# Performance work log

Hardware: AMD Instinct MI355X
Metric: run time of the kernel (lower is better)

The kernel has to match this reference:

```python
import jax, jax.numpy as jnp
import numpy as np

H, W_GRID = 64, 64          # grid size -> N = 4096 stations
CTX, HID = 512, 2048        # ctx_features, hidden_size
K, BATCH = 8, 8             # nearest_k, batch
N = H * W_GRID


def _build_neighbors(seed=0):
    """Mimics __init__: for each grid cell, k nearest cells by Euclidean grid
    distance, with similarity exp(-||f_i - f_j||) from a random scalar field."""
    rng = np.random.default_rng(seed)
    field = rng.standard_normal((H, W_GRID)).astype(np.float32)
    ii, jj = np.meshgrid(np.arange(H), np.arange(W_GRID), indexing='ij')
    coords = np.stack([ii.ravel(), jj.ravel()], axis=1).astype(np.float32)  # [N,2]
    d2 = ((coords[:, None, :] - coords[None, :, :]) ** 2).sum(-1).astype(np.float32)
    np.fill_diagonal(d2, np.inf)                      # exclude self (m!=i or n!=j)
    nn_idx = np.argsort(d2, axis=1)[:, :K].astype(np.int32)   # [N,K] flat ids
    f = field.ravel()
    sim = np.exp(-np.abs(f[:, None] - f[nn_idx])).astype(np.float32)  # [N,K]
    return nn_idx, sim


def setup_inputs() -> dict:
    key = jax.random.key(0)
    k1, k2 = jax.random.split(key)
    contextual_val = jax.random.normal(k1, (BATCH, H, W_GRID, CTX), dtype=jnp.float32)
    W = jax.random.normal(k2, (CTX, HID), dtype=jnp.float32)
    nn_idx, sim = _build_neighbors(seed=0)
    return {
        "contextual_val": contextual_val,
        "W": W,
        "nn_idx": jnp.asarray(nn_idx),
        "sim": jnp.asarray(sim),
    }


def reference(contextual_val, W, nn_idx, sim):
    # res[b, n, :] = sum_k sim[n, k] * (x[b, nn_idx[n, k], :] @ W)
    # By linearity: aggregate neighbor features with similarity weights first,
    # then apply the shared projection W once (same math, one GEMM).
    B = contextual_val.shape[0]
    x = contextual_val.reshape(B, N, CTX)          # [B, N, C]
    gathered = x[:, nn_idx]                        # [B, N, K, C] neighbor gather
    agg = jnp.einsum('nk,bnkc->bnc', sim, gathered)  # weighted scatter-add
    out = jnp.einsum('bnc,ch->bnh', agg, W)          # shared small matmul
    return out.reshape(B, H, W_GRID, HID)
```

## Files before the change

kernel.cpp:

```cpp
#include <hip/hip_runtime.h>
#include <cstdint>

#define CTX 512
#define HID 2048
#define NCELL 4096
#define M_TOT 32768

typedef __bf16 bf16;
typedef __attribute__((ext_vector_type(8))) __bf16 bf16x8;
typedef __attribute__((ext_vector_type(4))) float f32x4;

__device__ __align__(16) unsigned short g_agg[(size_t)M_TOT * CTX];
__device__ __align__(16) unsigned short g_WT[(size_t)HID * CTX];
__device__ int g_flag;

__device__ __forceinline__ float bf2f(unsigned short u) {
  union { unsigned int i; float f; } c; c.i = ((unsigned int)u) << 16; return c.f;
}
__device__ __forceinline__ unsigned short f2bf(float f) {
  union { float f; unsigned int i; } c; c.f = f;
  unsigned int u = c.i;
  u += 0x7fffu + ((u >> 16) & 1u);
  return (unsigned short)(u >> 16);
}
__device__ __forceinline__ float lo16(unsigned int w) {
  union { unsigned int i; float f; } c; c.i = w << 16; return c.f;
}
__device__ __forceinline__ float hi16(unsigned int w) {
  union { unsigned int i; float f; } c; c.i = w & 0xffff0000u; return c.f;
}

__device__ __forceinline__ void gload_lds16(const void* g, void* s) {
  __builtin_amdgcn_global_load_lds(
      (const __attribute__((address_space(1))) void*)g,
      (__attribute__((address_space(3))) void*)s, 16, 0, 0);
}

__global__ void detect_dtype(const unsigned short* __restrict__ x, int* flagp) {
  __shared__ int cnt;
  if (threadIdx.x == 0) cnt = 0;
  __syncthreads();
  const uint4 v = ((const uint4*)x)[threadIdx.x];
  unsigned int w[4] = {v.x, v.y, v.z, v.w};
  int c = 0;
#pragma unroll
  for (int i = 0; i < 4; ++i) {
    unsigned int lo = w[i] & 0xffffu, hi = w[i] >> 16;
    c += (((lo >> 7) & 0xffu) >= 0xF8u);
    c += (((hi >> 7) & 0xffu) >= 0xF8u);
  }
  atomicAdd(&cnt, c);
  __syncthreads();
  if (threadIdx.x == 0) *flagp = (cnt > 8) ? 1 : 0;
}

__global__ void transpose_w(const void* __restrict__ Wv,
                            unsigned short* __restrict__ wt,
                            const int* __restrict__ flagp) {
  const int isf32 = *flagp;
  const int t  = threadIdx.x;
  const int h  = blockIdx.x * 64 + (t & 63);
  const int c0 = (blockIdx.y * 4 + (t >> 6)) * 8;
  float e[8];
  if (isf32) {
    const float* Wf = (const float*)Wv;
#pragma unroll
    for (int j = 0; j < 8; ++j) e[j] = Wf[(size_t)(c0 + j) * HID + h];
  } else {
    const unsigned short* Wb = (const unsigned short*)Wv;
#pragma unroll
    for (int j = 0; j < 8; ++j) e[j] = bf2f(Wb[(size_t)(c0 + j) * HID + h]);
  }
  uint4 o;
  o.x = (unsigned int)f2bf(e[0]) | ((unsigned int)f2bf(e[1]) << 16);
  o.y = (unsigned int)f2bf(e[2]) | ((unsigned int)f2bf(e[3]) << 16);
  o.z = (unsigned int)f2bf(e[4]) | ((unsigned int)f2bf(e[5]) << 16);
  o.w = (unsigned int)f2bf(e[6]) | ((unsigned int)f2bf(e[7]) << 16);
  *(uint4*)&wt[(size_t)h * CTX + c0] = o;
}

__global__ void gather_agg_k(const void* __restrict__ xv,
                             const int* __restrict__ nn_idx,
                             const void* __restrict__ simv,
                             unsigned short* __restrict__ agg,
                             const int* __restrict__ flagp) {
  const int isf32 = *flagp;
  const int bid  = blockIdx.x;
  const int sb   = (bid & 7) * 1024 + (bid >> 3);
  const int m    = sb * 4 + (threadIdx.x >> 6);
  const int lane = threadIdx.x & 63;
  const int b    = m >> 12;
  const int n    = m & (NCELL - 1);

  float a[8] = {0, 0, 0, 0, 0, 0, 0, 0};
  if (isf32) {
    const int clo = lane * 4;
    const int chi = 256 + lane * 4;
    const float* xf = (const float*)xv;
    const float* sf = (const float*)simv;
#pragma unroll
    for (int k = 0; k < 8; ++k) {
      const int   idx = nn_idx[n * 8 + k];
      const float wgt = sf[n * 8 + k];
      const float* p  = xf + (size_t)(b * NCELL + idx) * CTX;
      const float4 v0 = *(const float4*)(p + clo);
      const float4 v1 = *(const float4*)(p + chi);
      a[0] += wgt * v0.x; a[1] += wgt * v0.y; a[2] += wgt * v0.z; a[3] += wgt * v0.w;
      a[4] += wgt * v1.x; a[5] += wgt * v1.y; a[6] += wgt * v1.z; a[7] += wgt * v1.w;
    }
    uint2 olo, ohi;
    olo.x = (unsigned int)f2bf(a[0]) | ((unsigned int)f2bf(a[1]) << 16);
    olo.y = (unsigned int)f2bf(a[2]) | ((unsigned int)f2bf(a[3]) << 16);
    ohi.x = (unsigned int)f2bf(a[4]) | ((unsigned int)f2bf(a[5]) << 16);
    ohi.y = (unsigned int)f2bf(a[6]) | ((unsigned int)f2bf(a[7]) << 16);
    *(uint2*)&agg[(size_t)m * CTX + clo] = olo;
    *(uint2*)&agg[(size_t)m * CTX + chi] = ohi;
  } else {
    const int c0 = lane * 8;
    const unsigned short* xb = (const unsigned short*)xv;
    const unsigned short* sb16 = (const unsigned short*)simv;
#pragma unroll
    for (int k = 0; k < 8; ++k) {
      const int   idx = nn_idx[n * 8 + k];
      const float wgt = bf2f(sb16[n * 8 + k]);
      const uint4 v = *(const uint4*)(xb + ((size_t)(b * NCELL + idx) * CTX + c0));
      a[0] += wgt * lo16(v.x); a[1] += wgt * hi16(v.x);
      a[2] += wgt * lo16(v.y); a[3] += wgt * hi16(v.y);
      a[4] += wgt * lo16(v.z); a[5] += wgt * hi16(v.z);
      a[6] += wgt * lo16(v.w); a[7] += wgt * hi16(v.w);
    }
    uint4 o;
    o.x = (unsigned int)f2bf(a[0]) | ((unsigned int)f2bf(a[1]) << 16);
    o.y = (unsigned int)f2bf(a[2]) | ((unsigned int)f2bf(a[3]) << 16);
    o.z = (unsigned int)f2bf(a[4]) | ((unsigned int)f2bf(a[5]) << 16);
    o.w = (unsigned int)f2bf(a[6]) | ((unsigned int)f2bf(a[7]) << 16);
    *(uint4*)&agg[(size_t)m * CTX + c0] = o;
  }
}

#define CS_STR 132
__global__ __launch_bounds__(256) void gemm_bt(const unsigned short* __restrict__ agg,
                                               const unsigned short* __restrict__ wt,
                                               void* __restrict__ outv,
                                               const int* __restrict__ flagp) {
  __shared__ __align__(16) char smem[65536];
  float* Cs = (float*)smem;

  const int tid  = threadIdx.x;
  const int wave = tid >> 6;
  const int lane = tid & 63;
  const int l16  = lane & 15;
  const int quad = lane >> 4;

  const int bid = blockIdx.x;
  const int swz = (bid & 7) * 512 + (bid >> 3);
  const int gn0 = (swz & 15) * 128;
  const int gm0 = (swz >> 4) * 128;

  const int wm = (wave & 1) * 64;
  const int wn = (wave >> 1) * 64;

  f32x4 acc[4][4] = {};

  const int srow = lane >> 3;
  const int l8   = lane & 7;

#define STAGE(b, kt)                                                          \
  {                                                                           \
    bf16* As_ = (bf16*)(smem + (b) * 32768);                                  \
    bf16* Bs_ = (bf16*)(smem + (b) * 32768 + 16384);                          \
    _Pragma("unroll")                                                         \
    for (int i = 0; i < 4; ++i) {                                             \
      const int chunk = wave * 4 + i;                                         \
      const int row   = chunk * 8 + srow;                                     \
      const int csw   = (l8 * 8) ^ ((row & 7) << 3);                          \
      gload_lds16(&agg[(size_t)(gm0 + row) * CTX + (kt) + csw],               \
                  &As_[chunk * 512]);                                         \
      gload_lds16(&wt[(size_t)(gn0 + row) * CTX + (kt) + csw],                \
                  &Bs_[chunk * 512]);                                         \
    }                                                                         \
  }

  STAGE(0, 0);

  for (int t = 0; t < 8; ++t) {
    if (t < 7) {
      STAGE((t + 1) & 1, (t + 1) * 64);
      asm volatile("s_waitcnt vmcnt(8)" ::: "memory");
    } else {
      asm volatile("s_waitcnt vmcnt(0)" ::: "memory");
    }
    __builtin_amdgcn_s_barrier();
    __builtin_amdgcn_sched_barrier(0);

    const bf16* A = (const bf16*)(smem + (t & 1) * 32768);
    const bf16* B = (const bf16*)(smem + (t & 1) * 32768 + 16384);

#pragma unroll
    for (int s = 0; s < 2; ++s) {
      bf16x8 af[4], bfr[4];
#pragma unroll
      for (int mi = 0; mi < 4; ++mi) {
        const int r = wm + mi * 16 + l16;
        af[mi] = *(const bf16x8*)&A[r * 64 + (((s * 4 + quad) * 8) ^ ((r & 7) << 3))];
      }
#pragma unroll
      for (int ni = 0; ni < 4; ++ni) {
        const int r = wn + ni * 16 + l16;
        bfr[ni] = *(const bf16x8*)&B[r * 64 + (((s * 4 + quad) * 8) ^ ((r & 7) << 3))];
      }
      __builtin_amdgcn_s_setprio(1);
#pragma unroll
      for (int mi = 0; mi < 4; ++mi)
#pragma unroll
        for (int ni = 0; ni < 4; ++ni)
          acc[mi][ni] = __builtin_amdgcn_mfma_f32_16x16x32_bf16(
              af[mi], bfr[ni], acc[mi][ni], 0, 0, 0);
      __builtin_amdgcn_s_setprio(0);
    }
    __builtin_amdgcn_s_barrier();
    __builtin_amdgcn_sched_barrier(0);
  }
#undef STAGE

  const int isf32 = *flagp;
  if (isf32) {
    float* out = (float*)outv;
#pragma unroll
    for (int h = 0; h < 2; ++h) {
      __syncthreads();
      if ((wave & 1) == h) {
#pragma unroll
        for (int mi = 0; mi < 4; ++mi)
#pragma unroll
          for (int r = 0; r < 4; ++r) {
            const int lr = mi * 16 + quad * 4 + r;
#pragma unroll
            for (int ni = 0; ni < 4; ++ni)
              Cs[lr * CS_STR + wn + ni * 16 + l16] = acc[mi][ni][r];
          }
      }
      __syncthreads();
#pragma unroll
      for (int p = 0; p < 8; ++p) {
        const int r  = p * 8 + (tid >> 5);
        const int c4 = (tid & 31) * 4;
        const f32x4 v = *(const f32x4*)&Cs[r * CS_STR + c4];
        *(f32x4*)&out[(size_t)(gm0 + h * 64 + r) * HID + gn0 + c4] = v;
      }
    }
  } else {
    unsigned short* out = (unsigned short*)outv;
#pragma unroll
    for (int mi = 0; mi < 4; ++mi)
#pragma unroll
      for (int r = 0; r < 4; ++r) {
        const size_t row = (size_t)(gm0 + wm + mi * 16 + quad * 4 + r);
#pragma unroll
        for (int ni = 0; ni < 4; ++ni)
          out[row * HID + gn0 + wn + ni * 16 + l16] = f2bf(acc[mi][ni][r]);
      }
  }
}

extern "C" void kernel_launch(void* const* d_in, const int* in_sizes, int n_in,
                              void* d_out, int out_size, void* d_ws, size_t ws_size,
                              hipStream_t stream) {
  const void* x   = d_in[0];
  const void* W   = d_in[1];
  const int*  nn  = (const int*)d_in[2];
  const void* sim = d_in[3];

  const size_t wt_bytes  = (size_t)HID * CTX * 2;
  const size_t agg_bytes = (size_t)M_TOT * CTX * 2;
  const size_t need      = wt_bytes + agg_bytes + 16;

  unsigned short *wt, *agg; int* flagp;
  if (ws_size >= need) {
    wt    = (unsigned short*)d_ws;
    agg   = (unsigned short*)((char*)d_ws + wt_bytes);
    flagp = (int*)((char*)d_ws + wt_bytes + agg_bytes);
  } else {
    void *p0, *p1, *p2;
    hipGetSymbolAddress(&p0, HIP_SYMBOL(g_WT));
    hipGetSymbolAddress(&p1, HIP_SYMBOL(g_agg));
    hipGetSymbolAddress(&p2, HIP_SYMBOL(g_flag));
    wt = (unsigned short*)p0; agg = (unsigned short*)p1; flagp = (int*)p2;
  }

  detect_dtype<<<1, 256, 0, stream>>>((const unsigned short*)x, flagp);
  transpose_w<<<dim3(HID / 64, CTX / 32), 256, 0, stream>>>(W, wt, flagp);
  gather_agg_k<<<dim3(M_TOT / 4), 256, 0, stream>>>(x, nn, sim, agg, flagp);
  gemm_bt<<<dim3((HID / 128) * (M_TOT / 128)), 256, 0, stream>>>(agg, wt, d_out, flagp);
}
```

Before: 405.6 us.

## Enlarge GEMM tile to 256x256 with 512 threads and interleaved prefetch

The bf16 MFMA GEMM moves from 128x128 tiles with 4 waves to 256x256 tiles with 8 waves, using 128 KB of dynamic LDS as two buffers. The aim is to raise arithmetic intensity and cut how often each block re-reads the agg and W tiles from global memory. Next-stage global-to-LDS loads are now split into four pieces and spread between MFMA groups, so memory traffic overlaps with compute. In exchange, 128 accumulator registers per lane and the large LDS footprint allow only one block per CU, and the grid shrinks to 1024 blocks, which may weaken latency hiding and leave a tail imbalance across CUs.

```diff
diff --git a/kernel.cpp b/kernel.cpp
--- a/kernel.cpp
+++ b/kernel.cpp
@@ -138,121 +138,123 @@
   }
 }
 
-#define CS_STR 132
-__global__ __launch_bounds__(256) void gemm_bt(const unsigned short* __restrict__ agg,
-                                               const unsigned short* __restrict__ wt,
-                                               void* __restrict__ outv,
-                                               const int* __restrict__ flagp) {
-  __shared__ __align__(16) char smem[65536];
-  float* Cs = (float*)smem;
+__global__ __launch_bounds__(512, 2) void gemm_bt(const unsigned short* __restrict__ agg,
+                                                  const unsigned short* __restrict__ wt,
+                                                  void* __restrict__ outv,
+                                                  const int* __restrict__ flagp) {
+  extern __shared__ char smem[];
 
   const int tid  = threadIdx.x;
   const int wave = tid >> 6;
   const int lane = tid & 63;
   const int l16  = lane & 15;
   const int quad = lane >> 4;
-
-  const int bid = blockIdx.x;
-  const int swz = (bid & 7) * 512 + (bid >> 3);
-  const int gn0 = (swz & 15) * 128;
-  const int gm0 = (swz >> 4) * 128;
-
-  const int wm = (wave & 1) * 64;
-  const int wn = (wave >> 1) * 64;
-
-  f32x4 acc[4][4] = {};
-
   const int srow = lane >> 3;
   const int l8   = lane & 7;
 
-#define STAGE(b, kt)                                                          \
+  const int bid = blockIdx.x;
+  const int swz = (bid & 7) * 128 + (bid >> 3);
+  const int gn0 = (swz & 7) * 256;
+  const int gm0 = (swz >> 3) * 256;
+
+  const int wm = (wave & 1) * 128;
+  const int wn = (wave >> 1) * 64;
+
+  f32x4 acc[8][4] = {};
+
+#define STAGE2(bsel, kt, j)                                                   \
   {                                                                           \
-    bf16* As_ = (bf16*)(smem + (b) * 32768);                                  \
-    bf16* Bs_ = (bf16*)(smem + (b) * 32768 + 16384);                          \
-    _Pragma("unroll")                                                         \
-    for (int i = 0; i < 4; ++i) {                                             \
-      const int chunk = wave * 4 + i;                                         \
-      const int row   = chunk * 8 + srow;                                     \
-      const int csw   = (l8 * 8) ^ ((row & 7) << 3);                          \
-      gload_lds16(&agg[(size_t)(gm0 + row) * CTX + (kt) + csw],               \
-                  &As_[chunk * 512]);                                         \
-      gload_lds16(&wt[(size_t)(gn0 + row) * CTX + (kt) + csw],                \
-                  &Bs_[chunk * 512]);                                         \
-    }                                                                         \
-  }
-
-  STAGE(0, 0);
+    const int chunk = wave * 4 + (j);                                         \
+    const int row   = chunk * 8 + srow;                                       \
+    const int csw   = (l8 * 8) ^ ((row & 7) << 3);                            \
+    gload_lds16(&agg[(size_t)(gm0 + row) * CTX + (kt) + csw],                 \
+                smem + (bsel) * 65536 + chunk * 1024);                        \
+    gload_lds16(&wt[(size_t)(gn0 + row) * CTX + (kt) + csw],                  \
+                smem + (bsel) * 65536 + 32768 + chunk * 1024);                \
+  }
+
+#pragma unroll
+  for (int j = 0; j < 4; ++j) STAGE2(0, 0, j);
 
   for (int t = 0; t < 8; ++t) {
-    if (t < 7) {
-      STAGE((t + 1) & 1, (t + 1) * 64);
-      asm volatile("s_waitcnt vmcnt(8)" ::: "memory");
-    } else {
-      asm volatile("s_waitcnt vmcnt(0)" ::: "memory");
-    }
+    const int c = t & 1;
+    __builtin_amdgcn_sched_barrier(0);
     __builtin_amdgcn_s_barrier();
     __builtin_amdgcn_sched_barrier(0);
-
-    const bf16* A = (const bf16*)(smem + (t & 1) * 32768);
-    const bf16* B = (const bf16*)(smem + (t & 1) * 32768 + 16384);
+    if (t < 7) STAGE2(c ^ 1, (t + 1) * 64, 0);
+    if (t < 7) asm volatile("s_waitcnt vmcnt(2)" ::: "memory");
+    else       asm volatile("s_waitcnt vmcnt(0)" ::: "memory");
+    __builtin_amdgcn_sched_barrier(0);
+    __builtin_amdgcn_s_barrier();
+    __builtin_amdgcn_sched_barrier(0);
+
+    const char* Ab = smem + c * 65536;
+    const char* Bb = Ab + 32768;
 
 #pragma unroll
     for (int s = 0; s < 2; ++s) {
-      bf16x8 af[4], bfr[4];
-#pragma unroll
-      for (int mi = 0; mi < 4; ++mi) {
-        const int r = wm + mi * 16 + l16;
-        af[mi] = *(const bf16x8*)&A[r * 64 + (((s * 4 + quad) * 8) ^ ((r & 7) << 3))];
-      }
+      bf16x8 bfv[4];
 #pragma unroll
       for (int ni = 0; ni < 4; ++ni) {
         const int r = wn + ni * 16 + l16;
-        bfr[ni] = *(const bf16x8*)&B[r * 64 + (((s * 4 + quad) * 8) ^ ((r & 7) << 3))];
-      }
-      __builtin_amdgcn_s_setprio(1);
-#pragma unroll
-      for (int mi = 0; mi < 4; ++mi)
-#pragma unroll
-        for (int ni = 0; ni < 4; ++ni)
-          acc[mi][ni] = __builtin_amdgcn_mfma_f32_16x16x32_bf16(
-              af[mi], bfr[ni], acc[mi][ni], 0, 0, 0);
-      __builtin_amdgcn_s_setprio(0);
+        bfv[ni] = *(const bf16x8*)(Bb + r * 128 +
+                                   2 * ((s * 32 + quad * 8) ^ ((r & 7) << 3)));
+      }
+#pragma unroll
+      for (int h = 0; h < 2; ++h) {
+        bf16x8 af[4];
+#pragma unroll
+        for (int mi2 = 0; mi2 < 4; ++mi2) {
+          const int r = wm + (h * 4 + mi2) * 16 + l16;
+          af[mi2] = *(const bf16x8*)(Ab + r * 128 +
+                                     2 * ((s * 32 + quad * 8) ^ ((r & 7) << 3)));
+        }
+        if (t < 7 && (s * 2 + h) < 3) STAGE2(c ^ 1, (t + 1) * 64, s * 2 + h + 1);
+        __builtin_amdgcn_s_setprio(1);
+#pragma unroll
+        for (int mi2 = 0; mi2 < 4; ++mi2)
+#pragma unroll
+          for (int ni = 0; ni < 4; ++ni)
+            acc[h * 4 + mi2][ni] = __builtin_amdgcn_mfma_f32_16x16x32_bf16(
+                af[mi2], bfv[ni], acc[h * 4 + mi2][ni], 0, 0, 0);
+        __builtin_amdgcn_s_setprio(0);
+      }
     }
-    __builtin_amdgcn_s_barrier();
-    __builtin_amdgcn_sched_barrier(0);
-  }
-#undef STAGE
+  }
+#undef STAGE2
 
   const int isf32 = *flagp;
   if (isf32) {
     float* out = (float*)outv;
-#pragma unroll
-    for (int h = 0; h < 2; ++h) {
+    float* Cs  = (float*)smem;
+#pragma unroll
+    for (int q = 0; q < 4; ++q) {
       __syncthreads();
-      if ((wave & 1) == h) {
-#pragma unroll
-        for (int mi = 0; mi < 4; ++mi)
+      if ((wave & 1) == (q >> 1)) {
+#pragma unroll
+        for (int mi2 = 0; mi2 < 4; ++mi2)
 #pragma unroll
           for (int r = 0; r < 4; ++r) {
-            const int lr = mi * 16 + quad * 4 + r;
+            const int lr = mi2 * 16 + quad * 4 + r;
 #pragma unroll
             for (int ni = 0; ni < 4; ++ni)
-              Cs[lr * CS_STR + wn + ni * 16 + l16] = acc[mi][ni][r];
+              Cs[lr * 260 + wn + ni * 16 + l16] = acc[(q & 1) * 4 + mi2][ni][r];
           }
       }
       __syncthreads();
 #pragma unroll
-      for (int p = 0; p < 8; ++p) {
-        const int r  = p * 8 + (tid >> 5);
-        const int c4 = (tid & 31) * 4;
-        const f32x4 v = *(const f32x4*)&Cs[r * CS_STR + c4];
-        *(f32x4*)&out[(size_t)(gm0 + h * 64 + r) * HID + gn0 + c4] = v;
+      for (int j = 0; j < 8; ++j) {
+        const int i  = j * 512 + tid;
+        const int r  = i >> 6;
+        const int c4 = (i & 63) * 4;
+        const f32x4 v = *(const f32x4*)&Cs[r * 260 + c4];
+        *(f32x4*)&out[(size_t)(gm0 + q * 64 + r) * HID + gn0 + c4] = v;
       }
     }
   } else {
     unsigned short* out = (unsigned short*)outv;
 #pragma unroll
-    for (int mi = 0; mi < 4; ++mi)
+    for (int mi = 0; mi < 8; ++mi)
 #pragma unroll
       for (int r = 0; r < 4; ++r) {
         const size_t row = (size_t)(gm0 + wm + mi * 16 + quad * 4 + r);
@@ -288,8 +290,15 @@
     wt = (unsigned short*)p0; agg = (unsigned short*)p1; flagp = (int*)p2;
   }
 
+  static int attr_done = 0;
+  if (!attr_done) {
+    hipFuncSetAttribute(reinterpret_cast<const void*>(&gemm_bt),
+                        hipFuncAttributeMaxDynamicSharedMemorySize, 131072);
+    attr_done = 1;
+  }
+
   detect_dtype<<<1, 256, 0, stream>>>((const unsigned short*)x, flagp);
   transpose_w<<<dim3(HID / 64, CTX / 32), 256, 0, stream>>>(W, wt, flagp);
   gather_agg_k<<<dim3(M_TOT / 4), 256, 0, stream>>>(x, nn, sim, agg, flagp);
-  gemm_bt<<<dim3((HID / 128) * (M_TOT / 128)), 256, 0, stream>>>(agg, wt, d_out, flagp);
-}
+  gemm_bt<<<dim3((HID / 256) * (M_TOT / 256)), 512, 131072, stream>>>(agg, wt, d_out, flagp);
+}
```

Result: no change. 401.0 us (-1.1%).
